# Performance work log

Measured on AMD Instinct MI355X. Metric: run time of the kernel, lower is better.

## Reference

```python
import jax, jax.numpy as jnp
import numpy as np

B, C, N, H = 4, 256, 4096, 4
DK = C // H


def _proj(x, w, b):
    # Conv1d with kernel size 1 == per-point linear: [B,C,N] x [O,C] -> [B,O,N]
    return jnp.einsum('oc,bcn->bon', w, x) + b[None, :, None]


def setup_inputs() -> dict:
    key = jax.random.key(0)
    ks = jax.random.split(key, 9)
    s = 1.0 / np.sqrt(C)
    return {
        'x': jax.random.normal(ks[0], (B, C, N), jnp.float32),
        'wq': jax.random.normal(ks[1], (C, C), jnp.float32) * s,
        'bq': jax.random.normal(ks[2], (C,), jnp.float32) * 0.01,
        'wk': jax.random.normal(ks[3], (C, C), jnp.float32) * s,
        'bk': jax.random.normal(ks[4], (C,), jnp.float32) * 0.01,
        'wv': jax.random.normal(ks[5], (C, C), jnp.float32) * s,
        'bv': jax.random.normal(ks[6], (C,), jnp.float32) * 0.01,
        'wp': jax.random.normal(ks[7], (C, C), jnp.float32) * s,
        'bp': jax.random.normal(ks[8], (C,), jnp.float32) * 0.01,
    }


def reference(x, wq, bq, wk, bk, wv, bv, wp, bp):
    b, c, n = x.shape
    q = _proj(x, wq, bq).reshape(b, H, DK, n)
    k = _proj(x, wk, bk).reshape(b, H, DK, n)
    v = _proj(x, wv, bv).reshape(b, H, DK, n)
    scale = 1.0 / jnp.sqrt(jnp.asarray(DK, x.dtype))
    # scores over point pairs: [B,H,N,N]
    scores = jnp.einsum('bhdn,bhdm->bhnm', q, k) * scale
    attn = jax.nn.softmax(scores, axis=-1)
    out = jnp.einsum('bhnm,bhdm->bhdn', attn, v)  # [B,H,DK,N]
    out = out.reshape(b, c, n)
    out = _proj(out, wp, bp)
    return out + x
```

## Files before the change

### kernel.cpp

```cpp
#include <hip/hip_runtime.h>


#define BDIM 4
#define CDIM 256
#define NDIM 4096
#define HDIM 4
#define DKDIM 64
#define NQ   (BDIM * HDIM * NDIM)
#define NSPLIT 4
#define KPERZ (NDIM / NSPLIT)
#define QSCALE 0.18033688011112042f

typedef __bf16 bf16x8 __attribute__((ext_vector_type(8)));
typedef float f32x4 __attribute__((ext_vector_type(4)));
typedef short s16x4 __attribute__((ext_vector_type(4)));
typedef unsigned short u16;
typedef unsigned int u32;

__device__ __forceinline__ u16 f2bf(float f) {
  union { __bf16 h; u16 s; } u; u.h = (__bf16)f; return u.s;
}
__device__ __forceinline__ float bf2f(u16 v) {
  union { u32 u; float f; } x; x.u = (u32)v << 16; return x.f;
}
__device__ __forceinline__ u32 pk2(float a, float b) {
  return (u32)f2bf(a) | ((u32)f2bf(b) << 16);
}
__device__ __forceinline__ void gload16(const u16* g, u16* l) {
  __builtin_amdgcn_global_load_lds(
      (const __attribute__((address_space(1))) void*)g,
      (__attribute__((address_space(3))) void*)l, 16, 0, 0);
}

__global__ __launch_bounds__(256) void xt_kernel(
    const float* __restrict__ x, u16* __restrict__ xT)
{
  const int b = blockIdx.z, c0 = blockIdx.y * 64, n0 = blockIdx.x * 64;
  __shared__ __align__(16) float T[64][68];
  const int t = threadIdx.x;
  {
    const int cr = t >> 4, nc = (t & 15) * 4;
    #pragma unroll
    for (int ci = 0; ci < 4; ++ci) {
      const float4 v = *(const float4*)&x[((size_t)(b * CDIM + c0 + cr + ci * 16)) * NDIM + n0 + nc];
      *(float4*)&T[cr + ci * 16][nc] = v;
    }
  }
  __syncthreads();
  {
    const int n = t >> 2, g = t & 3;
    union { u16 u[16]; uint4 v[2]; } pk;
    #pragma unroll
    for (int u_ = 0; u_ < 16; ++u_) pk.u[u_] = f2bf(T[g * 16 + u_][n]);
    uint4* dst = (uint4*)&xT[((size_t)(b * NDIM + n0 + n)) * CDIM + c0 + g * 16];
    dst[0] = pk.v[0]; dst[1] = pk.v[1];
  }
}

__global__ __launch_bounds__(256, 4) void qkv_kernel(
    const u16* __restrict__ xT,
    const float* __restrict__ wq, const float* __restrict__ bq,
    const float* __restrict__ wk, const float* __restrict__ bk,
    const float* __restrict__ wv, const float* __restrict__ bv,
    u16* __restrict__ qT, u16* __restrict__ kT, u16* __restrict__ vB)
{
  const int b = blockIdx.z;
  const int p = blockIdx.y >> 1;
  const int o0 = (blockIdx.y & 1) * 128;
  const int n0 = blockIdx.x * 64;
  const float* wsel = (p == 0) ? wq : (p == 1) ? wk : wv;
  const float* bsel = (p == 0) ? bq : (p == 1) ? bk : bv;
  const float wscale = (p == 0) ? QSCALE : 1.0f;

  __shared__ __align__(16) u16 XTs[64][40];
  __shared__ __align__(16) u16 Ws[128][40];
  const int t = threadIdx.x, lane = t & 63, w = t >> 6;
  const int qd = lane >> 4, lm = lane & 15;
  const int sr = t >> 2, sg = (t & 3) * 8;
  const int r2 = t >> 1, g2 = (t & 1) * 16;

  const u16* xsrc = xT + ((size_t)(b * NDIM + n0 + sr)) * CDIM + sg;
  const float* wsrc = wsel + (size_t)(o0 + r2) * CDIM + g2;

  f32x4 acc[4][2];
  #pragma unroll
  for (int nt = 0; nt < 4; ++nt)
    #pragma unroll
    for (int j = 0; j < 2; ++j) acc[nt][j] = (f32x4){0.f, 0.f, 0.f, 0.f};

  for (int cs = 0; cs < 8; ++cs) {
    __syncthreads();
    *(uint4*)&XTs[sr][sg] = *(const uint4*)(xsrc + cs * 32);
    {
      const float4 w0 = *(const float4*)(wsrc + cs * 32);
      const float4 w1 = *(const float4*)(wsrc + cs * 32 + 4);
      const float4 w2 = *(const float4*)(wsrc + cs * 32 + 8);
      const float4 w3 = *(const float4*)(wsrc + cs * 32 + 12);
      union { u32 p[8]; uint4 v[2]; } pw;
      pw.p[0] = pk2(w0.x * wscale, w0.y * wscale);
      pw.p[1] = pk2(w0.z * wscale, w0.w * wscale);
      pw.p[2] = pk2(w1.x * wscale, w1.y * wscale);
      pw.p[3] = pk2(w1.z * wscale, w1.w * wscale);
      pw.p[4] = pk2(w2.x * wscale, w2.y * wscale);
      pw.p[5] = pk2(w2.z * wscale, w2.w * wscale);
      pw.p[6] = pk2(w3.x * wscale, w3.y * wscale);
      pw.p[7] = pk2(w3.z * wscale, w3.w * wscale);
      *(uint4*)&Ws[r2][g2]     = pw.v[0];
      *(uint4*)&Ws[r2][g2 + 8] = pw.v[1];
    }
    __syncthreads();
    bf16x8 xf[4], wf[2];
    #pragma unroll
    for (int nt = 0; nt < 4; ++nt) xf[nt] = *(const bf16x8*)&XTs[16 * nt + lm][qd * 8];
    #pragma unroll
    for (int j = 0; j < 2; ++j) wf[j] = *(const bf16x8*)&Ws[32 * w + 16 * j + lm][qd * 8];
    #pragma unroll
    for (int nt = 0; nt < 4; ++nt)
      #pragma unroll
      for (int j = 0; j < 2; ++j) {
        if (p < 2)
          acc[nt][j] = __builtin_amdgcn_mfma_f32_16x16x32_bf16(xf[nt], wf[j], acc[nt][j], 0, 0, 0);
        else
          acc[nt][j] = __builtin_amdgcn_mfma_f32_16x16x32_bf16(wf[j], xf[nt], acc[nt][j], 0, 0, 0);
      }
  }

  if (p < 2) {
    u16* out = (p == 0) ? qT : kT;
    #pragma unroll
    for (int j = 0; j < 2; ++j) {
      const int og = o0 + 32 * w + 16 * j + lm;
      const float bv2 = bsel[og] * wscale;
      #pragma unroll
      for (int nt = 0; nt < 4; ++nt)
        #pragma unroll
        for (int r = 0; r < 4; ++r) {
          const int n = n0 + 16 * nt + 4 * qd + r;
          out[((size_t)(b * NDIM + n)) * CDIM + og] = f2bf(acc[nt][j][r] + bv2);
        }
    }
  } else {
    #pragma unroll
    for (int j = 0; j < 2; ++j) {
      const float4 b4 = *(const float4*)&bsel[o0 + 32 * w + 16 * j + 4 * qd];
      const float bvr[4] = {b4.x, b4.y, b4.z, b4.w};
      #pragma unroll
      for (int nt = 0; nt < 4; ++nt)
        #pragma unroll
        for (int r = 0; r < 4; ++r) {
          const int og = o0 + 32 * w + 16 * j + 4 * qd + r;
          const int n = n0 + 16 * nt + lm;
          vB[((size_t)(b * CDIM + og)) * NDIM + n] = f2bf(acc[nt][j][r] + bvr[r]);
        }
    }
  }
}

__global__ __launch_bounds__(256, 4) void attn_kernel(
    const u16* __restrict__ qT, const u16* __restrict__ kT,
    const u16* __restrict__ vB, u16* __restrict__ Opart,
    float* __restrict__ Lp)
{
  const int bh = blockIdx.y, b = bh >> 2, h = bh & 3;
  const int n0 = blockIdx.x * 128;
  const int z  = blockIdx.z;

  __shared__ __align__(16) u16 KVlds[2][2][64][64];

  const int t = threadIdx.x, lane = t & 63, w = t >> 6;
  const int qd = lane >> 4, lm = lane & 15, l7 = lm & 7;

  bf16x8 qf[2][2];
  {
    const u16* qbase = qT + ((size_t)(b * NDIM) + n0) * CDIM + h * 64;
    #pragma unroll
    for (int s = 0; s < 2; ++s)
      #pragma unroll
      for (int hh = 0; hh < 2; ++hh)
        qf[s][hh] = *(const bf16x8*)(qbase +
            (size_t)(16 * (2 * w + s) + lm) * CDIM + 32 * hh + qd * 8);
  }

  float l_i[2] = {0.f, 0.f};
  f32x4 oa[2][4];
  #pragma unroll
  for (int s = 0; s < 2; ++s)
    #pragma unroll
    for (int dt = 0; dt < 4; ++dt) oa[s][dt] = (f32x4){0.f, 0.f, 0.f, 0.f};

  const int srow = lane >> 3;
  const int swz  = 8 * ((lane & 7) ^ srow);
  const u16* kp0 = kT + ((size_t)(b * NDIM + z * KPERZ + 8 * w + srow)) * CDIM + h * 64 + swz;
  const u16* kp1 = kp0 + (size_t)32 * CDIM;
  const u16* vp0 = vB + ((size_t)(b * CDIM + h * 64 + 8 * w + srow)) * NDIM + z * KPERZ + swz;
  const u16* vp1 = vp0 + (size_t)32 * NDIM;

  {
    u16* kb = &KVlds[0][0][0][0];
    u16* vb2 = &KVlds[0][1][0][0];
    gload16(kp0, kb + w * 512);
    gload16(kp1, kb + (4 + w) * 512);
    gload16(vp0, vb2 + w * 512);
    gload16(vp1, vb2 + (4 + w) * 512);
  }

  #pragma unroll 1
  for (int it = 0; it < KPERZ / 64; ++it) {
    __syncthreads();
    if (it + 1 < KPERZ / 64) {
      const size_t ko = (size_t)(it + 1) * 64 * CDIM;
      const int    vo = (it + 1) * 64;
      u16* kb = &KVlds[(it + 1) & 1][0][0][0];
      u16* vb2 = &KVlds[(it + 1) & 1][1][0][0];
      gload16(kp0 + ko, kb + w * 512);
      gload16(kp1 + ko, kb + (4 + w) * 512);
      gload16(vp0 + vo, vb2 + w * 512);
      gload16(vp1 + vo, vb2 + (4 + w) * 512);
    }
    const u16 (*Kt)[64] = KVlds[it & 1][0];
    const u16 (*Vt)[64] = KVlds[it & 1][1];

    union { u16 u[4]; s16x4 v; } pk[2][4];
    float rs[2] = {0.f, 0.f};

    #pragma unroll
    for (int nt = 0; nt < 4; ++nt) {
      const bf16x8 kf0 = *(const bf16x8*)&Kt[16 * nt + lm][8 * (qd ^ l7)];
      const bf16x8 kf1 = *(const bf16x8*)&Kt[16 * nt + lm][8 * ((4 + qd) ^ l7)];
      #pragma unroll
      for (int s = 0; s < 2; ++s) {
        f32x4 zz = (f32x4){0.f, 0.f, 0.f, 0.f};
        zz = __builtin_amdgcn_mfma_f32_16x16x32_bf16(kf0, qf[s][0], zz, 0, 0, 0);
        zz = __builtin_amdgcn_mfma_f32_16x16x32_bf16(kf1, qf[s][1], zz, 0, 0, 0);
        #pragma unroll
        for (int r = 0; r < 4; ++r) {
          const float p = __builtin_amdgcn_exp2f(zz[r]);
          pk[s][nt].u[r] = f2bf(p);
          rs[s] += p;
        }
      }
    }
    l_i[0] += rs[0];
    l_i[1] += rs[1];

    #pragma unroll
    for (int c = 0; c < 4; ++c) {
      s16x4 av[4];
      #pragma unroll
      for (int dt = 0; dt < 4; ++dt)
        av[dt] = *(const s16x4*)&Vt[16 * dt + lm][(16 * c + 4 * qd) ^ (8 * l7)];
      #pragma unroll
      for (int dt = 0; dt < 4; ++dt) {
        oa[0][dt] = __builtin_amdgcn_mfma_f32_16x16x16bf16_1k(av[dt], pk[0][c].v, oa[0][dt], 0, 0, 0);
        oa[1][dt] = __builtin_amdgcn_mfma_f32_16x16x16bf16_1k(av[dt], pk[1][c].v, oa[1][dt], 0, 0, 0);
      }
    }
  }

  #pragma unroll
  for (int s = 0; s < 2; ++s) {
    l_i[s] += __shfl_xor(l_i[s], 16);
    l_i[s] += __shfl_xor(l_i[s], 32);
  }

  __syncthreads();
  u16 (*Ot)[72] = (u16(*)[72])&KVlds[0][0][0][0];
  #pragma unroll
  for (int s = 0; s < 2; ++s) {
    const float inv = 1.0f / l_i[s];
    #pragma unroll
    for (int dt = 0; dt < 4; ++dt)
      #pragma unroll
      for (int r = 0; r < 4; ++r)
        Ot[16 * (2 * w + s) + lm][16 * dt + 4 * qd + r] = f2bf(oa[s][dt][r] * inv);
  }
  if (qd == 0) {
    const size_t lbase = ((size_t)z * (BDIM * HDIM) + bh) * NDIM;
    #pragma unroll
    for (int s = 0; s < 2; ++s)
      Lp[lbase + n0 + 16 * (2 * w + s) + lm] = l_i[s];
  }
  __syncthreads();
  {
    const int r = t >> 1, g = (t & 1) * 32;
    u16* dst = Opart + (((size_t)z * (BDIM * HDIM) + bh) * NDIM + n0 + r) * DKDIM + g;
    const uint4* srcp = (const uint4*)&Ot[r][g];
    uint4* d4 = (uint4*)dst;
    d4[0] = srcp[0]; d4[1] = srcp[1]; d4[2] = srcp[2]; d4[3] = srcp[3];
  }
}

__global__ __launch_bounds__(256, 4) void projout_kernel(
    const u16* __restrict__ Opart, const float* __restrict__ Lp,
    const float* __restrict__ wp, const float* __restrict__ bp,
    const float* __restrict__ res, float* __restrict__ out)
{
  const int b = blockIdx.z, o0 = blockIdx.y * 128, n0 = blockIdx.x * 64;
  __shared__ __align__(16) u16 XTs[64][40];
  __shared__ __align__(16) u16 Ws[128][40];
  const int t = threadIdx.x, lane = t & 63, w = t >> 6;
  const int qd = lane >> 4, lm = lane & 15;
  const int sr = t >> 2, sg = (t & 3) * 8;
  const int r2 = t >> 1, g2 = (t & 1) * 16;

  float wh[4][NSPLIT];
  #pragma unroll
  for (int hh = 0; hh < 4; ++hh) {
    const size_t i0 = ((size_t)(b * HDIM + hh)) * NDIM + n0 + sr;
    float l[NSPLIT], tot = 0.f;
    #pragma unroll
    for (int zz = 0; zz < NSPLIT; ++zz) { l[zz] = Lp[(size_t)zz * NQ + i0]; tot += l[zz]; }
    const float iv = 1.0f / tot;
    #pragma unroll
    for (int zz = 0; zz < NSPLIT; ++zz) wh[hh][zz] = l[zz] * iv;
  }

  const float* wsrc = wp + (size_t)(o0 + r2) * CDIM + g2;

  f32x4 acc[4][2];
  #pragma unroll
  for (int nt = 0; nt < 4; ++nt)
    #pragma unroll
    for (int j = 0; j < 2; ++j) acc[nt][j] = (f32x4){0.f, 0.f, 0.f, 0.f};

  for (int cs = 0; cs < 8; ++cs) {
    const int c0 = cs * 32;
    const int hh = c0 >> 6;
    const int dk = (c0 & 63) + sg;
    __syncthreads();
    {
      const size_t obase = (((size_t)(b * HDIM + hh)) * NDIM + n0 + sr) * DKDIM + dk;
      float v[8] = {0.f, 0.f, 0.f, 0.f, 0.f, 0.f, 0.f, 0.f};
      #pragma unroll
      for (int zz = 0; zz < NSPLIT; ++zz) {
        union { u16 u[8]; uint4 q; } a;
        a.q = *(const uint4*)(Opart + (size_t)zz * NQ * DKDIM + obase);
        const float wz = wh[hh][zz];
        #pragma unroll
        for (int j = 0; j < 8; ++j) v[j] = fmaf(wz, bf2f(a.u[j]), v[j]);
      }
      union { u16 u[8]; uint4 q; } ov;
      #pragma unroll
      for (int j = 0; j < 8; ++j) ov.u[j] = f2bf(v[j]);
      *(uint4*)&XTs[sr][sg] = ov.q;
      const float4 wv0 = *(const float4*)(wsrc + c0);
      const float4 wv1 = *(const float4*)(wsrc + c0 + 4);
      const float4 wv2 = *(const float4*)(wsrc + c0 + 8);
      const float4 wv3 = *(const float4*)(wsrc + c0 + 12);
      union { u32 p[8]; uint4 v[2]; } pw;
      pw.p[0] = pk2(wv0.x, wv0.y); pw.p[1] = pk2(wv0.z, wv0.w);
      pw.p[2] = pk2(wv1.x, wv1.y); pw.p[3] = pk2(wv1.z, wv1.w);
      pw.p[4] = pk2(wv2.x, wv2.y); pw.p[5] = pk2(wv2.z, wv2.w);
      pw.p[6] = pk2(wv3.x, wv3.y); pw.p[7] = pk2(wv3.z, wv3.w);
      *(uint4*)&Ws[r2][g2]     = pw.v[0];
      *(uint4*)&Ws[r2][g2 + 8] = pw.v[1];
    }
    __syncthreads();
    bf16x8 xf[4], wf[2];
    #pragma unroll
    for (int nt = 0; nt < 4; ++nt) xf[nt] = *(const bf16x8*)&XTs[16 * nt + lm][qd * 8];
    #pragma unroll
    for (int j = 0; j < 2; ++j) wf[j] = *(const bf16x8*)&Ws[32 * w + 16 * j + lm][qd * 8];
    #pragma unroll
    for (int nt = 0; nt < 4; ++nt)
      #pragma unroll
      for (int j = 0; j < 2; ++j)
        acc[nt][j] = __builtin_amdgcn_mfma_f32_16x16x32_bf16(wf[j], xf[nt], acc[nt][j], 0, 0, 0);
  }

  #pragma unroll
  for (int j = 0; j < 2; ++j) {
    const float4 b4 = *(const float4*)&bp[o0 + 32 * w + 16 * j + 4 * qd];
    const float bvr[4] = {b4.x, b4.y, b4.z, b4.w};
    #pragma unroll
    for (int nt = 0; nt < 4; ++nt)
      #pragma unroll
      for (int r = 0; r < 4; ++r) {
        const int og = o0 + 32 * w + 16 * j + 4 * qd + r;
        const int n = n0 + 16 * nt + lm;
        const size_t idx = ((size_t)(b * CDIM + og)) * NDIM + n;
        out[idx] = acc[nt][j][r] + bvr[r] + res[idx];
      }
  }
}

extern "C" void kernel_launch(void* const* d_in, const int* in_sizes, int n_in,
                              void* d_out, int out_size, void* d_ws, size_t ws_size,
                              hipStream_t stream)
{
  const float* x  = (const float*)d_in[0];
  const float* wq = (const float*)d_in[1];
  const float* bq = (const float*)d_in[2];
  const float* wk = (const float*)d_in[3];
  const float* bk = (const float*)d_in[4];
  const float* wv = (const float*)d_in[5];
  const float* bv = (const float*)d_in[6];
  const float* wp = (const float*)d_in[7];
  const float* bp = (const float*)d_in[8];
  float* out = (float*)d_out;

  const size_t sz = (size_t)BDIM * CDIM * NDIM;
  u16* xTb = (u16*)d_ws;
  u16* qTb = xTb + sz;
  u16* kTb = qTb + sz;
  u16* vBb = kTb + sz;
  u16* Opart = vBb + sz;
  float* Lp = (float*)(Opart + (size_t)NSPLIT * sz);

  const dim3 blk(256);
  xt_kernel<<<dim3(NDIM / 64, CDIM / 64, BDIM), blk, 0, stream>>>(x, xTb);
  qkv_kernel<<<dim3(NDIM / 64, 6, BDIM), blk, 0, stream>>>(
      xTb, wq, bq, wk, bk, wv, bv, qTb, kTb, vBb);
  attn_kernel<<<dim3(NDIM / 128, BDIM * HDIM, NSPLIT), blk, 0, stream>>>(
      qTb, kTb, vBb, Opart, Lp);
  projout_kernel<<<dim3(NDIM / 64, 2, BDIM), blk, 0, stream>>>(
      Opart, Lp, wp, bp, x, out);
}
```

Before: 202.2 us.

## Pre-convert weights to bf16 once and cut attention key-split to two

Adds a small kernel that converts all four weight matrices (with the query scale folded in) to bf16 up front. The projection kernels then load MFMA weight fragments straight from global memory instead of re-converting fp32 weights and staging them through LDS in every block. Separately, the attention key split drops from four to two, which halves the partial-output traffic and the merge work in the output projection but gives the attention kernel fewer blocks to spread across the GPU. The extra launch and the direct global fragment loads could offset some of the savings.

```diff
diff --git a/kernel.cpp b/kernel.cpp
--- a/kernel.cpp
+++ b/kernel.cpp
@@ -7,9 +7,10 @@
 #define HDIM 4
 #define DKDIM 64
 #define NQ   (BDIM * HDIM * NDIM)
-#define NSPLIT 4
+#define NSPLIT 2
 #define KPERZ (NDIM / NSPLIT)
 #define QSCALE 0.18033688011112042f
+#define WSZ (CDIM * CDIM)
 
 typedef __bf16 bf16x8 __attribute__((ext_vector_type(8)));
 typedef float f32x4 __attribute__((ext_vector_type(4)));
@@ -32,6 +33,25 @@
       (__attribute__((address_space(3))) void*)l, 16, 0, 0);
 }
 
+__global__ __launch_bounds__(256) void wconv_kernel(
+    const float* __restrict__ wq, const float* __restrict__ wk,
+    const float* __restrict__ wv, const float* __restrict__ wp,
+    u16* __restrict__ wb)
+{
+  const int a = blockIdx.y;
+  const float* src = (a == 0) ? wq : (a == 1) ? wk : (a == 2) ? wv : wp;
+  const float sc = (a == 0) ? QSCALE : 1.0f;
+  const int i = (blockIdx.x * 256 + threadIdx.x) * 8;
+  const float4 v0 = *(const float4*)(src + i);
+  const float4 v1 = *(const float4*)(src + i + 4);
+  union { u32 p[4]; uint4 q; } o;
+  o.p[0] = pk2(v0.x * sc, v0.y * sc);
+  o.p[1] = pk2(v0.z * sc, v0.w * sc);
+  o.p[2] = pk2(v1.x * sc, v1.y * sc);
+  o.p[3] = pk2(v1.z * sc, v1.w * sc);
+  *(uint4*)(wb + (size_t)a * WSZ + i) = o.q;
+}
+
 __global__ __launch_bounds__(256) void xt_kernel(
     const float* __restrict__ x, u16* __restrict__ xT)
 {
@@ -58,29 +78,26 @@
 }
 
 __global__ __launch_bounds__(256, 4) void qkv_kernel(
-    const u16* __restrict__ xT,
-    const float* __restrict__ wq, const float* __restrict__ bq,
-    const float* __restrict__ wk, const float* __restrict__ bk,
-    const float* __restrict__ wv, const float* __restrict__ bv,
+    const u16* __restrict__ xT, const u16* __restrict__ wb,
+    const float* __restrict__ bq, const float* __restrict__ bk,
+    const float* __restrict__ bv,
     u16* __restrict__ qT, u16* __restrict__ kT, u16* __restrict__ vB)
 {
   const int b = blockIdx.z;
   const int p = blockIdx.y >> 1;
   const int o0 = (blockIdx.y & 1) * 128;
   const int n0 = blockIdx.x * 64;
-  const float* wsel = (p == 0) ? wq : (p == 1) ? wk : wv;
   const float* bsel = (p == 0) ? bq : (p == 1) ? bk : bv;
   const float wscale = (p == 0) ? QSCALE : 1.0f;
 
   __shared__ __align__(16) u16 XTs[64][40];
-  __shared__ __align__(16) u16 Ws[128][40];
   const int t = threadIdx.x, lane = t & 63, w = t >> 6;
   const int qd = lane >> 4, lm = lane & 15;
   const int sr = t >> 2, sg = (t & 3) * 8;
-  const int r2 = t >> 1, g2 = (t & 1) * 16;
 
   const u16* xsrc = xT + ((size_t)(b * NDIM + n0 + sr)) * CDIM + sg;
-  const float* wsrc = wsel + (size_t)(o0 + r2) * CDIM + g2;
+  const u16* wrow0 = wb + (size_t)p * WSZ + (size_t)(o0 + 32 * w + lm) * CDIM + qd * 8;
+  const u16* wrow1 = wrow0 + (size_t)16 * CDIM;
 
   f32x4 acc[4][2];
   #pragma unroll
@@ -89,40 +106,24 @@
     for (int j = 0; j < 2; ++j) acc[nt][j] = (f32x4){0.f, 0.f, 0.f, 0.f};
 
   for (int cs = 0; cs < 8; ++cs) {
+    const bf16x8 wf0 = *(const bf16x8*)(wrow0 + cs * 32);
+    const bf16x8 wf1 = *(const bf16x8*)(wrow1 + cs * 32);
     __syncthreads();
     *(uint4*)&XTs[sr][sg] = *(const uint4*)(xsrc + cs * 32);
-    {
-      const float4 w0 = *(const float4*)(wsrc + cs * 32);
-      const float4 w1 = *(const float4*)(wsrc + cs * 32 + 4);
-      const float4 w2 = *(const float4*)(wsrc + cs * 32 + 8);
-      const float4 w3 = *(const float4*)(wsrc + cs * 32 + 12);
-      union { u32 p[8]; uint4 v[2]; } pw;
-      pw.p[0] = pk2(w0.x * wscale, w0.y * wscale);
-      pw.p[1] = pk2(w0.z * wscale, w0.w * wscale);
-      pw.p[2] = pk2(w1.x * wscale, w1.y * wscale);
-      pw.p[3] = pk2(w1.z * wscale, w1.w * wscale);
-      pw.p[4] = pk2(w2.x * wscale, w2.y * wscale);
-      pw.p[5] = pk2(w2.z * wscale, w2.w * wscale);
-      pw.p[6] = pk2(w3.x * wscale, w3.y * wscale);
-      pw.p[7] = pk2(w3.z * wscale, w3.w * wscale);
-      *(uint4*)&Ws[r2][g2]     = pw.v[0];
-      *(uint4*)&Ws[r2][g2 + 8] = pw.v[1];
-    }
     __syncthreads();
-    bf16x8 xf[4], wf[2];
+    bf16x8 xf[4];
     #pragma unroll
     for (int nt = 0; nt < 4; ++nt) xf[nt] = *(const bf16x8*)&XTs[16 * nt + lm][qd * 8];
     #pragma unroll
-    for (int j = 0; j < 2; ++j) wf[j] = *(const bf16x8*)&Ws[32 * w + 16 * j + lm][qd * 8];
-    #pragma unroll
-    for (int nt = 0; nt < 4; ++nt)
-      #pragma unroll
-      for (int j = 0; j < 2; ++j) {
-        if (p < 2)
-          acc[nt][j] = __builtin_amdgcn_mfma_f32_16x16x32_bf16(xf[nt], wf[j], acc[nt][j], 0, 0, 0);
-        else
-          acc[nt][j] = __builtin_amdgcn_mfma_f32_16x16x32_bf16(wf[j], xf[nt], acc[nt][j], 0, 0, 0);
+    for (int nt = 0; nt < 4; ++nt) {
+      if (p < 2) {
+        acc[nt][0] = __builtin_amdgcn_mfma_f32_16x16x32_bf16(xf[nt], wf0, acc[nt][0], 0, 0, 0);
+        acc[nt][1] = __builtin_amdgcn_mfma_f32_16x16x32_bf16(xf[nt], wf1, acc[nt][1], 0, 0, 0);
+      } else {
+        acc[nt][0] = __builtin_amdgcn_mfma_f32_16x16x32_bf16(wf0, xf[nt], acc[nt][0], 0, 0, 0);
+        acc[nt][1] = __builtin_amdgcn_mfma_f32_16x16x32_bf16(wf1, xf[nt], acc[nt][1], 0, 0, 0);
       }
+    }
   }
 
   if (p < 2) {
@@ -292,16 +293,14 @@
 
 __global__ __launch_bounds__(256, 4) void projout_kernel(
     const u16* __restrict__ Opart, const float* __restrict__ Lp,
-    const float* __restrict__ wp, const float* __restrict__ bp,
+    const u16* __restrict__ wb, const float* __restrict__ bp,
     const float* __restrict__ res, float* __restrict__ out)
 {
   const int b = blockIdx.z, o0 = blockIdx.y * 128, n0 = blockIdx.x * 64;
   __shared__ __align__(16) u16 XTs[64][40];
-  __shared__ __align__(16) u16 Ws[128][40];
   const int t = threadIdx.x, lane = t & 63, w = t >> 6;
   const int qd = lane >> 4, lm = lane & 15;
   const int sr = t >> 2, sg = (t & 3) * 8;
-  const int r2 = t >> 1, g2 = (t & 1) * 16;
 
   float wh[4][NSPLIT];
   #pragma unroll
@@ -315,7 +314,8 @@
     for (int zz = 0; zz < NSPLIT; ++zz) wh[hh][zz] = l[zz] * iv;
   }
 
-  const float* wsrc = wp + (size_t)(o0 + r2) * CDIM + g2;
+  const u16* wrow0 = wb + (size_t)3 * WSZ + (size_t)(o0 + 32 * w + lm) * CDIM + qd * 8;
+  const u16* wrow1 = wrow0 + (size_t)16 * CDIM;
 
   f32x4 acc[4][2];
   #pragma unroll
@@ -327,6 +327,8 @@
     const int c0 = cs * 32;
     const int hh = c0 >> 6;
     const int dk = (c0 & 63) + sg;
+    const bf16x8 wf0 = *(const bf16x8*)(wrow0 + c0);
+    const bf16x8 wf1 = *(const bf16x8*)(wrow1 + c0);
     __syncthreads();
     {
       const size_t obase = (((size_t)(b * HDIM + hh)) * NDIM + n0 + sr) * DKDIM + dk;
@@ -343,29 +345,16 @@
       #pragma unroll
       for (int j = 0; j < 8; ++j) ov.u[j] = f2bf(v[j]);
       *(uint4*)&XTs[sr][sg] = ov.q;
-      const float4 wv0 = *(const float4*)(wsrc + c0);
-      const float4 wv1 = *(const float4*)(wsrc + c0 + 4);
-      const float4 wv2 = *(const float4*)(wsrc + c0 + 8);
-      const float4 wv3 = *(const float4*)(wsrc + c0 + 12);
-      union { u32 p[8]; uint4 v[2]; } pw;
-      pw.p[0] = pk2(wv0.x, wv0.y); pw.p[1] = pk2(wv0.z, wv0.w);
-      pw.p[2] = pk2(wv1.x, wv1.y); pw.p[3] = pk2(wv1.z, wv1.w);
-      pw.p[4] = pk2(wv2.x, wv2.y); pw.p[5] = pk2(wv2.z, wv2.w);
-      pw.p[6] = pk2(wv3.x, wv3.y); pw.p[7] = pk2(wv3.z, wv3.w);
-      *(uint4*)&Ws[r2][g2]     = pw.v[0];
-      *(uint4*)&Ws[r2][g2 + 8] = pw.v[1];
     }
     __syncthreads();
-    bf16x8 xf[4], wf[2];
+    bf16x8 xf[4];
     #pragma unroll
     for (int nt = 0; nt < 4; ++nt) xf[nt] = *(const bf16x8*)&XTs[16 * nt + lm][qd * 8];
     #pragma unroll
-    for (int j = 0; j < 2; ++j) wf[j] = *(const bf16x8*)&Ws[32 * w + 16 * j + lm][qd * 8];
-    #pragma unroll
-    for (int nt = 0; nt < 4; ++nt)
-      #pragma unroll
-      for (int j = 0; j < 2; ++j)
-        acc[nt][j] = __builtin_amdgcn_mfma_f32_16x16x32_bf16(wf[j], xf[nt], acc[nt][j], 0, 0, 0);
+    for (int nt = 0; nt < 4; ++nt) {
+      acc[nt][0] = __builtin_amdgcn_mfma_f32_16x16x32_bf16(wf0, xf[nt], acc[nt][0], 0, 0, 0);
+      acc[nt][1] = __builtin_amdgcn_mfma_f32_16x16x32_bf16(wf1, xf[nt], acc[nt][1], 0, 0, 0);
+    }
   }
 
   #pragma unroll
@@ -406,13 +395,15 @@
   u16* vBb = kTb + sz;
   u16* Opart = vBb + sz;
   float* Lp = (float*)(Opart + (size_t)NSPLIT * sz);
+  u16* wbf = (u16*)(Lp + (size_t)NSPLIT * NQ);
 
   const dim3 blk(256);
+  wconv_kernel<<<dim3(WSZ / (256 * 8), 4, 1), blk, 0, stream>>>(wq, wk, wv, wp, wbf);
   xt_kernel<<<dim3(NDIM / 64, CDIM / 64, BDIM), blk, 0, stream>>>(x, xTb);
   qkv_kernel<<<dim3(NDIM / 64, 6, BDIM), blk, 0, stream>>>(
-      xTb, wq, bq, wk, bk, wv, bv, qTb, kTb, vBb);
+      xTb, wbf, bq, bk, bv, qTb, kTb, vBb);
   attn_kernel<<<dim3(NDIM / 128, BDIM * HDIM, NSPLIT), blk, 0, stream>>>(
       qTb, kTb, vBb, Opart, Lp);
   projout_kernel<<<dim3(NDIM / 64, 2, BDIM), blk, 0, stream>>>(
-      Opart, Lp, wp, bp, x, out);
-}
+      Opart, Lp, wbf, bp, x, out);
+}
```

After: 198.3 us. Within noise of the previous version (-1.9%).
